# Kernel tuning notes

Hardware: AMD Instinct MI355X
Metric: run time of the kernel (lower is better)

Reference implementation:

```python
import jax, jax.numpy as jnp
import numpy as np

# dims: batch, seq_len, d_model, heads, head_dim, n_buckets
B, L, DM, H, DH, K = 4, 4096, 1024, 16, 64, 8
C = L // K            # chunk length after bucket sort (512); extra_len==0 for these dims
CS = 0.1              # cluster_score mixing weight


def setup_inputs() -> dict:
    key = jax.random.key(0)
    ks = jax.random.split(key, 12)
    s = 0.02
    def p(k, shape):
        return jax.random.normal(k, shape, jnp.float32) * s
    return {
        "inputs_q": jax.random.normal(ks[0], (B, L, DM), jnp.float32),
        "wq": p(ks[1], (DM, H, DH)), "bq": jnp.zeros((H, DH), jnp.float32),
        "wk": p(ks[2], (DM, H, DH)), "bk": jnp.zeros((H, DH), jnp.float32),
        "wv": p(ks[3], (DM, H, DH)), "bv": jnp.zeros((H, DH), jnp.float32),
        "w_shared": p(ks[4], (H, DH, K)),
        "w_qscore": p(ks[5], (H, DH, K)),
        "w_kscore": p(ks[6], (H, DH, K)),
        "wo": p(ks[7], (H, DH, DM)), "bo": jnp.zeros((DM,), jnp.float32),
    }


def reference(inputs_q, wq, bq, wk, bk, wv, bv, w_shared, w_qscore, w_kscore, wo, bo):
    scale = 1.0 / np.sqrt(DH)
    # QKV projections (DenseGeneral to (H, DH))
    q = jnp.einsum('bld,dhk->blhk', inputs_q, wq) + bq  # [B,L,H,DH]
    k = jnp.einsum('bld,dhk->blhk', inputs_q, wk) + bk
    v = jnp.einsum('bld,dhk->blhk', inputs_q, wv) + bv

    # learned linear cluster scores on stop-gradient q/k
    mix_q = (1.0 - CS) * w_shared + CS * w_qscore  # [H,DH,K]
    mix_k = (1.0 - CS) * w_shared + CS * w_kscore
    qs = jnp.einsum('blhd,hdk->blhk', jax.lax.stop_gradient(q), mix_q)  # [B,L,H,K]
    ksc = jnp.einsum('blhd,hdk->blhk', jax.lax.stop_gradient(k), mix_k)

    # bucket assignment = argmax learned score; per-(batch,head) stable sort by bucket id
    bq_id = jnp.argmax(qs, -1).transpose(0, 2, 1)   # [B,H,L]
    bk_id = jnp.argmax(ksc, -1).transpose(0, 2, 1)
    sort_q = jnp.argsort(bq_id, axis=-1)            # stable in jax
    sort_k = jnp.argsort(bk_id, axis=-1)

    qh = q.transpose(0, 2, 1, 3)  # [B,H,L,DH]
    kh = k.transpose(0, 2, 1, 3)
    vh = v.transpose(0, 2, 1, 3)
    sq = jnp.take_along_axis(qh, sort_q[..., None], axis=2).reshape(B, H, K, C, DH)
    sk = jnp.take_along_axis(kh, sort_k[..., None], axis=2).reshape(B, H, K, C, DH)
    sv = jnp.take_along_axis(vh, sort_k[..., None], axis=2).reshape(B, H, K, C, DH)

    # block attention within each bucket chunk
    logits = jnp.einsum('bhncd,bhned->bhnce', sq, sk) * scale  # [B,H,K,C,C]
    attn = jax.nn.softmax(logits, axis=-1)
    o = jnp.einsum('bhnce,bhned->bhncd', attn, sv).reshape(B, H, L, DH)

    # unsort back to original token order
    inv_q = jnp.argsort(sort_q, axis=-1)
    o = jnp.take_along_axis(o, inv_q[..., None], axis=2)  # [B,H,L,DH]
    o = o.transpose(0, 2, 1, 3)                            # [B,L,H,DH]

    out = jnp.einsum('blhd,hdo->blo', o, wo) + bo          # output projection

    # auxiliary load-balancing routing loss over buckets (extra_loss)
    p_q = jax.nn.softmax(qs, -1)
    p_k = jax.nn.softmax(ksc, -1)
    f_q = jax.nn.one_hot(jnp.argmax(qs, -1), K, dtype=qs.dtype)
    f_k = jax.nn.one_hot(jnp.argmax(ksc, -1), K, dtype=qs.dtype)
    lq = K * jnp.mean(jnp.sum(jnp.mean(f_q, 1) * jnp.mean(p_q, 1), -1))
    lk = K * jnp.mean(jnp.sum(jnp.mean(f_k, 1) * jnp.mean(p_k, 1), -1))
    extra_loss = 0.5 * (lq + lk)
    return out, extra_loss
```

## Files before the change

kernel.cpp:

```cpp
#include <hip/hip_runtime.h>
#include <hip/hip_bf16.h>

#define BB 4
#define LL 4096
#define DM 1024
#define HH 16
#define DHD 64
#define KB 8
#define BL 16384
#define FLAGCAP 131072

typedef __attribute__((ext_vector_type(8))) short short8;
typedef __attribute__((ext_vector_type(4))) short short4v;
typedef __attribute__((ext_vector_type(4))) float float4v;

#define MFMA16(A, Bx, C) __builtin_amdgcn_mfma_f32_16x16x32_bf16(A, Bx, C, 0, 0, 0)

static __device__ __forceinline__ short bf16s(float f) {
  __hip_bfloat16 h = __float2bfloat16(f);
  return *reinterpret_cast<short*>(&h);
}
static __device__ __forceinline__ float b2f(short s) {
  __hip_bfloat16 h = *reinterpret_cast<__hip_bfloat16*>(&s);
  return __bfloat162float(h);
}
static __device__ __forceinline__ void gl16(const void* g, void* l) {
  __builtin_amdgcn_global_load_lds(
      (const __attribute__((address_space(1))) void*)g,
      (__attribute__((address_space(3))) void*)l, 16, 0, 0);
}

__global__ __launch_bounds__(256) void xcvt(const float* __restrict__ x,
                                            __hip_bfloat16* __restrict__ xb) {
  int i = (blockIdx.x * 256 + threadIdx.x) * 8;
  float4 f0 = *reinterpret_cast<const float4*>(x + i);
  float4 f1 = *reinterpret_cast<const float4*>(x + i + 4);
  short8 o;
  o[0] = bf16s(f0.x); o[1] = bf16s(f0.y); o[2] = bf16s(f0.z); o[3] = bf16s(f0.w);
  o[4] = bf16s(f1.x); o[5] = bf16s(f1.y); o[6] = bf16s(f1.z); o[7] = bf16s(f1.w);
  *reinterpret_cast<short8*>(xb + i) = o;
}

__global__ __launch_bounds__(256) void prep_wt(const float* __restrict__ wq,
                                               const float* __restrict__ wk,
                                               const float* __restrict__ wv,
                                               const float* __restrict__ wo,
                                               __hip_bfloat16* __restrict__ wt_qkv,
                                               __hip_bfloat16* __restrict__ wt_o) {
  int blk = blockIdx.x;
  int s = blk >> 8;
  int rem = blk & 255;
  int k0 = (rem >> 4) * 64;
  int n0 = (rem & 15) * 64;
  const float* src = (s == 0) ? wq : (s == 1) ? wk : (s == 2) ? wv : wo;
  __hip_bfloat16* dst = (s < 3) ? (wt_qkv + (size_t)s * 1024 * 1024) : wt_o;
  __shared__ float ls[64][65];
  int t = threadIdx.x;
#pragma unroll
  for (int p = 0; p < 4; ++p) {
    int sid = p * 256 + t;
    int r = sid >> 4, c4 = sid & 15;
    float4 v = *reinterpret_cast<const float4*>(src + (size_t)(k0 + r) * 1024 + n0 + c4 * 4);
    ls[r][c4 * 4 + 0] = v.x; ls[r][c4 * 4 + 1] = v.y;
    ls[r][c4 * 4 + 2] = v.z; ls[r][c4 * 4 + 3] = v.w;
  }
  __syncthreads();
#pragma unroll
  for (int p = 0; p < 4; ++p) {
    int sid = p * 256 + t;
    int n = sid >> 4, kq = sid & 15;
    short4v pk;
#pragma unroll
    for (int j = 0; j < 4; ++j) pk[j] = bf16s(ls[kq * 4 + j][n]);
    *reinterpret_cast<short4v*>(dst + (size_t)(n0 + n) * 1024 + k0 + kq * 4) = pk;
  }
}

__global__ __launch_bounds__(256) void prep_wsc(const float* __restrict__ wq,
                                                const float* __restrict__ wk,
                                                const float* __restrict__ wsh,
                                                const float* __restrict__ wqs,
                                                const float* __restrict__ wks,
                                                const float* __restrict__ bq,
                                                const float* __restrict__ bk,
                                                double* __restrict__ wscg,
                                                double* __restrict__ bsc,
                                                __hip_bfloat16* __restrict__ whb,
                                                __hip_bfloat16* __restrict__ wmb) {
  int col = blockIdx.x;
  int side = col >> 7, h = (col >> 3) & 15, kk = col & 7;
  int g = side * 16 + h;
  const float* w = side ? wk : wq;
  const float* wscore = side ? wks : wqs;
  __shared__ double mix[64];
  int t = threadIdx.x;
  if (t < 64)
    mix[t] = 0.9 * (double)wsh[(h * 64 + t) * 8 + kk] +
             0.1 * (double)wscore[(h * 64 + t) * 8 + kk];
  __syncthreads();
#pragma unroll
  for (int p = 0; p < 4; ++p) {
    int d = p * 256 + t;
    double acc = 0.0;
    const float* wr = w + (size_t)d * 1024 + h * 64;
#pragma unroll
    for (int j = 0; j < 64; ++j) acc += (double)wr[j] * mix[j];
    wscg[((size_t)g * 1024 + d) * 8 + kk] = acc;
    short hi = bf16s((float)acc);
    short mid = bf16s((float)(acc - (double)b2f(hi)));
    *reinterpret_cast<short*>(whb + (size_t)col * 1024 + d) = hi;
    *reinterpret_cast<short*>(wmb + (size_t)col * 1024 + d) = mid;
  }
  if (t == 0) {
    const float* br = (side ? bk : bq) + h * 64;
    double acc = 0.0;
    for (int j = 0; j < 64; ++j) acc += (double)br[j] * mix[j];
    bsc[col] = acc;
  }
}

__global__ __launch_bounds__(256) void score_gemm(const float* __restrict__ x,
                                                  const __hip_bfloat16* __restrict__ whb,
                                                  const __hip_bfloat16* __restrict__ wmb,
                                                  const double* __restrict__ bsc,
                                                  float* __restrict__ S2) {
  __shared__ char sm[49152];
  int t = threadIdx.x;
  int m0 = blockIdx.x * 64;
  int n0 = blockIdx.y * 128;
  int lane = t & 63;
  int wu = __builtin_amdgcn_readfirstlane(t >> 6);
  int lm = lane & 15, quad = lane >> 4;
  int wmr = (wu & 1) * 32, wn = (wu >> 1) * 64;
  int rb = wu * 32, rr = lane >> 3, phys = lane & 7;
  float4v zero = {0.f, 0.f, 0.f, 0.f};
  float4v acc[2][4];
#pragma unroll
  for (int i = 0; i < 2; ++i)
#pragma unroll
    for (int j = 0; j < 4; ++j) acc[i][j] = zero;

  for (int k0 = 0; k0 < 1024; k0 += 64) {
    __syncthreads();
#pragma unroll
    for (int p = 0; p < 2; ++p) {
      int sid = p * 256 + t;
      int m = sid >> 3, kc = sid & 7;
      const float* ap = x + (size_t)(m0 + m) * 1024 + k0 + kc * 8;
      float4 f0 = *reinterpret_cast<const float4*>(ap);
      float4 f1 = *reinterpret_cast<const float4*>(ap + 4);
      float vv[8] = {f0.x, f0.y, f0.z, f0.w, f1.x, f1.y, f1.z, f1.w};
      short8 hi, lo;
#pragma unroll
      for (int e = 0; e < 8; ++e) {
        short h = bf16s(vv[e]);
        hi[e] = h;
        lo[e] = bf16s(vv[e] - b2f(h));
      }
      *reinterpret_cast<short8*>(sm + m * 128 + ((kc + m) & 7) * 16) = hi;
      *reinterpret_cast<short8*>(sm + 8192 + m * 128 + ((kc + m) & 7) * 16) = lo;
    }
#pragma unroll
    for (int p = 0; p < 4; ++p) {
      int row = rb + p * 8 + rr;
      int kc = (phys - row) & 7;
      gl16(whb + (size_t)(n0 + row) * 1024 + k0 + kc * 8, sm + 16384 + (rb + p * 8) * 128);
      gl16(wmb + (size_t)(n0 + row) * 1024 + k0 + kc * 8, sm + 32768 + (rb + p * 8) * 128);
    }
    __syncthreads();
#pragma unroll
    for (int kh = 0; kh < 2; ++kh) {
      short8 ah[2], al[2], bh[4], bm[4];
#pragma unroll
      for (int i = 0; i < 2; ++i) {
        int row = wmr + i * 16 + lm;
        int ph = ((kh * 4 + quad) + row) & 7;
        ah[i] = *reinterpret_cast<const short8*>(sm + row * 128 + ph * 16);
        al[i] = *reinterpret_cast<const short8*>(sm + 8192 + row * 128 + ph * 16);
      }
#pragma unroll
      for (int j = 0; j < 4; ++j) {
        int rn = wn + j * 16 + lm;
        int ph = ((kh * 4 + quad) + rn) & 7;
        bh[j] = *reinterpret_cast<const short8*>(sm + 16384 + rn * 128 + ph * 16);
        bm[j] = *reinterpret_cast<const short8*>(sm + 32768 + rn * 128 + ph * 16);
      }
#pragma unroll
      for (int i = 0; i < 2; ++i)
#pragma unroll
        for (int j = 0; j < 4; ++j) {
          acc[i][j] = MFMA16(ah[i], bh[j], acc[i][j]);
          acc[i][j] = MFMA16(ah[i], bm[j], acc[i][j]);
          acc[i][j] = MFMA16(al[i], bh[j], acc[i][j]);
        }
    }
  }

#pragma unroll
  for (int i = 0; i < 2; ++i)
#pragma unroll
    for (int j = 0; j < 4; ++j) {
      int n = n0 + wn + j * 16 + lm;
      float bias = (float)bsc[n];
#pragma unroll
      for (int r = 0; r < 4; ++r) {
        int row = m0 + wmr + i * 16 + quad * 4 + r;
        S2[(size_t)(n >> 3) * 131072 + row * 8 + (n & 7)] = acc[i][j][r] + bias;
      }
    }
}

__global__ __launch_bounds__(512) void bucket_kernel(const float* __restrict__ S2,
                                                     int* __restrict__ bid,
                                                     float* __restrict__ psumg,
                                                     int* __restrict__ flagcnt,
                                                     int* __restrict__ list) {
  int t = threadIdx.x;
  int lane = t & 63;
  int w = t >> 6;
  int T0 = blockIdx.x * 64;
  int tg = T0 + lane;
  int b = tg >> 12, l = tg & 4095;
#pragma unroll
  for (int gi = 0; gi < 4; ++gi) {
    int g = gi * 8 + w;
    const float* sp = S2 + (size_t)g * 131072 + tg * 8;
    float4 v0 = *reinterpret_cast<const float4*>(sp);
    float4 v1 = *reinterpret_cast<const float4*>(sp + 4);
    float v[8] = {v0.x, v0.y, v0.z, v0.w, v1.x, v1.y, v1.z, v1.w};
    float mx = v[0]; int am = 0;
#pragma unroll
    for (int j = 1; j < 8; ++j) { if (v[j] > mx) { mx = v[j]; am = j; } }
    float mx2 = -3.0e38f;
#pragma unroll
    for (int j = 0; j < 8; ++j) { if (j != am && v[j] > mx2) mx2 = v[j]; }
    int side = g >> 4, h = g & 15;
    int slab = (side * 4 + b) * 16 + h;
    bid[(slab << 12) | l] = am;
    if (mx - mx2 < 5e-4f) {
      int pos = atomicAdd(flagcnt, 1);
      if (pos < FLAGCAP) list[pos] = (slab << 12) | l;
    }
    float es = 0.f, e[8];
#pragma unroll
    for (int j = 0; j < 8; ++j) { e[j] = __expf(v[j] - mx); es += e[j]; }
    float inv = 1.f / es;
#pragma unroll
    for (int j = 0; j < 8; ++j) {
      float s = e[j] * inv;
      s += __shfl_xor(s, 1);  s += __shfl_xor(s, 2);  s += __shfl_xor(s, 4);
      s += __shfl_xor(s, 8);  s += __shfl_xor(s, 16); s += __shfl_xor(s, 32);
      if (lane == 0) atomicAdd(&psumg[slab * 8 + j], s);
    }
  }
}

__global__ __launch_bounds__(256) void refine_kernel(const float* __restrict__ x,
                                                     const double* __restrict__ wscg,
                                                     const double* __restrict__ bsc,
                                                     const int* __restrict__ flagcnt,
                                                     const int* __restrict__ list,
                                                     int* __restrict__ bid) {
  int lane = threadIdx.x & 63;
  int w = threadIdx.x >> 6;
  int cnt = flagcnt[0];
  if (cnt > FLAGCAP) cnt = FLAGCAP;
  for (int i = blockIdx.x * 4 + w; i < cnt; i += 1024) {
    int e = list[i];
    int slab = e >> 12, l = e & 4095;
    int side = slab >> 6, b = (slab >> 4) & 3, h = slab & 15;
    int g = side * 16 + h;
    int row = b * 4096 + l;
    double acc[8] = {0, 0, 0, 0, 0, 0, 0, 0};
    const float* xr = x + (size_t)row * 1024 + lane * 16;
    const double* wr = wscg + ((size_t)g * 1024 + lane * 16) * 8;
#pragma unroll
    for (int dd = 0; dd < 16; ++dd) {
      double xv = (double)xr[dd];
#pragma unroll
      for (int j = 0; j < 8; ++j) acc[j] += xv * wr[dd * 8 + j];
    }
#pragma unroll
    for (int j = 0; j < 8; ++j) {
      double v = acc[j];
      v += __shfl_xor(v, 32); v += __shfl_xor(v, 16); v += __shfl_xor(v, 8);
      v += __shfl_xor(v, 4);  v += __shfl_xor(v, 2);  v += __shfl_xor(v, 1);
      acc[j] = v + bsc[g * 8 + j];
    }
    if (lane == 0) {
      double mx = acc[0]; int am = 0;
#pragma unroll
      for (int j = 1; j < 8; ++j) { if (acc[j] > mx) { mx = acc[j]; am = j; } }
      bid[(slab << 12) | l] = am;
    }
  }
}

__global__ __launch_bounds__(256) void sort_kernel(const int* __restrict__ bid,
                                                   int* __restrict__ sortq,
                                                   int* __restrict__ sortk,
                                                   int* __restrict__ cntg) {
  int blk = blockIdx.x;
  int side = blk >> 6, b = (blk >> 4) & 3, h = blk & 15;
  const int* ids = bid + (((side * 4 + b) * 16 + h) << 12);
  int* outp = (side ? sortk : sortq) + ((b * 16 + h) << 12);
  __shared__ int cnt[8][257];
  __shared__ int base[8];
  int t = threadIdx.x;
  int loc[16];
  int hist[8] = {0, 0, 0, 0, 0, 0, 0, 0};
#pragma unroll
  for (int j = 0; j < 16; ++j) { loc[j] = ids[t * 16 + j] & 7; hist[loc[j]]++; }
#pragma unroll
  for (int k = 0; k < 8; ++k) cnt[k][t + 1] = hist[k];
  if (t < 8) cnt[t][0] = 0;
  __syncthreads();
  if (t < 8) {
    for (int i = 1; i <= 256; ++i) cnt[t][i] += cnt[t][i - 1];
  }
  __syncthreads();
  if (t == 0) {
    int run = 0;
    for (int k = 0; k < 8; ++k) { base[k] = run; run += cnt[k][256]; }
  }
  if (t < 8) cntg[((side * 4 + b) * 16 + h) * 8 + t] = cnt[t][256];
  __syncthreads();
#pragma unroll
  for (int j = 0; j < 16; ++j) {
    int k = loc[j];
    int before = 0;
#pragma unroll
    for (int i = 0; i < 16; ++i) before += (i < j && loc[i] == k) ? 1 : 0;
    int pos = base[k] + cnt[k][t] + before;
    outp[pos] = t * 16 + j;
  }
}

template <bool CBF16>
__global__ __launch_bounds__(256) void gemm_k(const __hip_bfloat16* __restrict__ A,
                                              const __hip_bfloat16* __restrict__ Bt,
                                              void* __restrict__ Cv,
                                              const float* __restrict__ b0,
                                              const float* __restrict__ b1,
                                              const float* __restrict__ b2,
                                              int nblk) {
  __shared__ char sm[32768];
  int t = threadIdx.x;
  int blk = blockIdx.x;
  int m0 = (blk / nblk) * 128;
  int n0 = (blk % nblk) * 128;
  int lane = t & 63;
  int wu = __builtin_amdgcn_readfirstlane(t >> 6);
  int lm = lane & 15, quad = lane >> 4;
  int wm = (wu & 1) * 64, wn = (wu >> 1) * 64;
  int rb = wu * 32, rr = lane >> 3, phys = lane & 7;
  float4v zero = {0.f, 0.f, 0.f, 0.f};
  float4v acc[4][4];
#pragma unroll
  for (int i = 0; i < 4; ++i)
#pragma unroll
    for (int j = 0; j < 4; ++j) acc[i][j] = zero;

  for (int k0 = 0; k0 < 1024; k0 += 64) {
    __syncthreads();
#pragma unroll
    for (int p = 0; p < 4; ++p) {
      int row = rb + p * 8 + rr;
      int kc = (phys - row) & 7;
      gl16(A + (size_t)(m0 + row) * 1024 + k0 + kc * 8, sm + (rb + p * 8) * 128);
      gl16(Bt + (size_t)(n0 + row) * 1024 + k0 + kc * 8, sm + 16384 + (rb + p * 8) * 128);
    }
    __syncthreads();
#pragma unroll
    for (int kh = 0; kh < 2; ++kh) {
      short8 af[4], bf[4];
#pragma unroll
      for (int i = 0; i < 4; ++i) {
        int row = wm + i * 16 + lm;
        int ph = ((kh * 4 + quad) + row) & 7;
        af[i] = *reinterpret_cast<const short8*>(sm + row * 128 + ph * 16);
        int rn = wn + i * 16 + lm;
        int phb = ((kh * 4 + quad) + rn) & 7;
        bf[i] = *reinterpret_cast<const short8*>(sm + 16384 + rn * 128 + phb * 16);
      }
#pragma unroll
      for (int i = 0; i < 4; ++i)
#pragma unroll
        for (int j = 0; j < 4; ++j) acc[i][j] = MFMA16(af[i], bf[j], acc[i][j]);
    }
  }

  if constexpr (CBF16) {
    int s = n0 >> 10, nnb = n0 & 1023;
    const float* bias = (s == 0) ? b0 : (s == 1) ? b1 : b2;
    __hip_bfloat16* C = (__hip_bfloat16*)Cv + (size_t)s * BL * 1024;
#pragma unroll
    for (int i = 0; i < 4; ++i)
#pragma unroll
      for (int j = 0; j < 4; ++j) {
        int nn = nnb + wn + j * 16 + lm;
        float bvx = bias[nn];
#pragma unroll
        for (int r = 0; r < 4; ++r) {
          int row = m0 + wm + i * 16 + quad * 4 + r;
          C[(size_t)row * 1024 + nn] = __float2bfloat16(acc[i][j][r] + bvx);
        }
      }
  } else {
    float* C = (float*)Cv;
#pragma unroll
    for (int i = 0; i < 4; ++i)
#pragma unroll
      for (int j = 0; j < 4; ++j) {
        int gn = n0 + wn + j * 16 + lm;
        float bvx = b0[gn];
#pragma unroll
        for (int r = 0; r < 4; ++r) {
          int row = m0 + wm + i * 16 + quad * 4 + r;
          C[(size_t)row * 1024 + gn] = acc[i][j][r] + bvx;
        }
      }
  }
}

__global__ __launch_bounds__(256) void vt_kernel(const __hip_bfloat16* __restrict__ vb,
                                                 const int* __restrict__ sortk,
                                                 __hip_bfloat16* __restrict__ vT) {
  int cid = blockIdx.x;
  int b = cid >> 7, h = (cid >> 3) & 15, n = cid & 7;
  int sbase = ((b * 16 + h) << 12) + n * 512;
  __shared__ __hip_bfloat16 ls[64][72];
  int t = threadIdx.x;
  for (int kt = 0; kt < 8; ++kt) {
    __syncthreads();
#pragma unroll
    for (int p = 0; p < 2; ++p) {
      int sid = p * 256 + t;
      int key = sid >> 3, kc = sid & 7;
      int tok = sortk[sbase + kt * 64 + key];
      short8 v = *reinterpret_cast<const short8*>(vb + ((size_t)(b * 4096 + tok) * 16 + h) * 64 + kc * 8);
      *reinterpret_cast<short8*>(&ls[key][kc * 8]) = v;
    }
    __syncthreads();
#pragma unroll
    for (int p = 0; p < 2; ++p) {
      int sid = p * 256 + t;
      int dim = sid >> 3, kc = sid & 7;
      short8 o;
#pragma unroll
      for (int j = 0; j < 8; ++j) o[j] = *reinterpret_cast<short*>(&ls[kc * 8 + j][dim]);
      *reinterpret_cast<short8*>(vT + ((size_t)cid * 64 + dim) * 512 + kt * 64 + kc * 8) = o;
    }
  }
}

__global__ __launch_bounds__(256) void attn_kernel(const __hip_bfloat16* __restrict__ qb,
                                                   const __hip_bfloat16* __restrict__ kb,
                                                   const __hip_bfloat16* __restrict__ vT,
                                                   const int* __restrict__ sortq,
                                                   const int* __restrict__ sortk,
                                                   __hip_bfloat16* __restrict__ ao) {
  __shared__ char sm[25600];
  int t = threadIdx.x;
  int lane = t & 63, w = t >> 6;
  int lm = lane & 15, quad = lane >> 4;
  int cid = blockIdx.x >> 3, qt = blockIdx.x & 7;
  int b = cid >> 7, h = (cid >> 3) & 15, n = cid & 7;
  int sbase = (b * 16 + h) << 12;
  int psOff = 16384 + w * 2304;

  int qtok = sortq[sbase + n * 512 + qt * 64 + w * 16 + lm];
  const __hip_bfloat16* qp = qb + ((size_t)(b * 4096 + qtok) * 16 + h) * 64 + quad * 8;
  short8 aq0 = *reinterpret_cast<const short8*>(qp);
  short8 aq1 = *reinterpret_cast<const short8*>(qp + 32);

  float4v zero = {0.f, 0.f, 0.f, 0.f};
  float4v accO[4];
#pragma unroll
  for (int i = 0; i < 4; ++i) accO[i] = zero;
  float lsum[4] = {0.f, 0.f, 0.f, 0.f};

  for (int kt = 0; kt < 8; ++kt) {
    __syncthreads();
#pragma unroll
    for (int p = 0; p < 2; ++p) {
      int sid = p * 256 + t;
      int row = sid >> 3, kc = sid & 7;
      int tok = sortk[sbase + n * 512 + kt * 64 + row];
      short8 kv = *reinterpret_cast<const short8*>(kb + ((size_t)(b * 4096 + tok) * 16 + h) * 64 + kc * 8);
      *reinterpret_cast<short8*>(sm + row * 128 + ((kc + row) & 7) * 16) = kv;
      short8 vv = *reinterpret_cast<const short8*>(vT + ((size_t)cid * 64 + row) * 512 + kt * 64 + kc * 8);
      *reinterpret_cast<short8*>(sm + 8192 + row * 128 + ((kc + row) & 7) * 16) = vv;
    }
    __syncthreads();
#pragma unroll
    for (int nt = 0; nt < 4; ++nt) {
      int key = nt * 16 + lm;
      int ph0 = (quad + key) & 7;
      int ph1 = (4 + quad + key) & 7;
      short8 bk0 = *reinterpret_cast<const short8*>(sm + key * 128 + ph0 * 16);
      short8 bk1 = *reinterpret_cast<const short8*>(sm + key * 128 + ph1 * 16);
      float4v S = zero;
      S = MFMA16(aq0, bk0, S);
      S = MFMA16(aq1, bk1, S);
#pragma unroll
      for (int r = 0; r < 4; ++r) {
        float e = __expf(S[r] * 0.125f);
        lsum[r] += e;
        *reinterpret_cast<short*>(sm + psOff + (quad * 4 + r) * 144 + key * 2) = bf16s(e);
      }
    }
    __builtin_amdgcn_s_waitcnt(0);
#pragma unroll
    for (int ks = 0; ks < 2; ++ks) {
      short8 ap = *reinterpret_cast<const short8*>(sm + psOff + lm * 144 + ks * 64 + quad * 16);
#pragma unroll
      for (int dt = 0; dt < 4; ++dt) {
        int dim = dt * 16 + lm;
        int ph = (ks * 4 + quad + dim) & 7;
        short8 bv = *reinterpret_cast<const short8*>(sm + 8192 + dim * 128 + ph * 16);
        accO[dt] = MFMA16(ap, bv, accO[dt]);
      }
    }
  }
#pragma unroll
  for (int r = 0; r < 4; ++r) {
    float l = lsum[r];
    l += __shfl_xor(l, 1); l += __shfl_xor(l, 2);
    l += __shfl_xor(l, 4); l += __shfl_xor(l, 8);
    lsum[r] = 1.f / l;
  }
#pragma unroll
  for (int dt = 0; dt < 4; ++dt)
#pragma unroll
    for (int r = 0; r < 4; ++r)
      *reinterpret_cast<short*>(sm + psOff + (quad * 4 + r) * 144 + (dt * 16 + lm) * 2) =
          bf16s(accO[dt][r] * lsum[r]);
  __builtin_amdgcn_s_waitcnt(0);
  int q2 = lane >> 2, c = lane & 3;
  int tok2 = sortq[sbase + n * 512 + qt * 64 + w * 16 + q2];
  __hip_bfloat16* op = ao + ((size_t)(b * 4096 + tok2) * 16 + h) * 64;
  short8 o0 = *reinterpret_cast<const short8*>(sm + psOff + q2 * 144 + c * 16);
  short8 o1 = *reinterpret_cast<const short8*>(sm + psOff + q2 * 144 + (c + 4) * 16);
  *reinterpret_cast<short8*>(op + c * 8) = o0;
  *reinterpret_cast<short8*>(op + (c + 4) * 8) = o1;
}

__global__ __launch_bounds__(1024) void loss_kernel(const int* __restrict__ cntg,
                                                    const float* __restrict__ psumg,
                                                    float* __restrict__ out) {
  int t = threadIdx.x;
  float term = ((float)cntg[t] * (1.f / 4096.f)) * (psumg[t] * (1.f / 4096.f));
#pragma unroll
  for (int o = 1; o < 64; o <<= 1) term += __shfl_xor(term, o);
  __shared__ float wsum[16];
  if ((t & 63) == 0) wsum[t >> 6] = term;
  __syncthreads();
  if (t == 0) {
    float s = 0.f;
    for (int i = 0; i < 16; ++i) s += wsum[i];
    out[16777216] = s * (1.f / 16.f);
  }
}

extern "C" void kernel_launch(void* const* d_in, const int* in_sizes, int n_in,
                              void* d_out, int out_size, void* d_ws, size_t ws_size,
                              hipStream_t stream) {
  (void)in_sizes; (void)n_in; (void)out_size; (void)ws_size;
  const float* x   = (const float*)d_in[0];
  const float* wq  = (const float*)d_in[1];
  const float* bq  = (const float*)d_in[2];
  const float* wk  = (const float*)d_in[3];
  const float* bk  = (const float*)d_in[4];
  const float* wv  = (const float*)d_in[5];
  const float* bv  = (const float*)d_in[6];
  const float* wsh = (const float*)d_in[7];
  const float* wqs = (const float*)d_in[8];
  const float* wks = (const float*)d_in[9];
  const float* wo  = (const float*)d_in[10];
  const float* bo  = (const float*)d_in[11];

  char* ws = (char*)d_ws;
  __hip_bfloat16* wt_qkv = (__hip_bfloat16*)(ws + 0);
  __hip_bfloat16* wt_o   = (__hip_bfloat16*)(ws + 6291456);
  double* wscg  = (double*)(ws + 8388608);
  double* bsc   = (double*)(ws + 10485760);
  __hip_bfloat16* qkv  = (__hip_bfloat16*)(ws + 10487808);
  __hip_bfloat16* whb = (__hip_bfloat16*)(ws + 109051904);
  __hip_bfloat16* wmb = (__hip_bfloat16*)(ws + 109576192);
  int* flagcnt = (int*)(ws + 110100480);
  int* list    = (int*)(ws + 110100736);
  __hip_bfloat16* attn = (__hip_bfloat16*)(ws + 111151104);
  float* S2 = (float*)(ws + 111151104);
  int* bid    = (int*)(ws + 144705536);
  int* sortq  = (int*)(ws + 146802688);
  int* sortk  = (int*)(ws + 147851264);
  float* psumg = (float*)(ws + 148899840);
  int* cntg    = (int*)(ws + 148903936);
  __hip_bfloat16* vT = (__hip_bfloat16*)d_out;
  __hip_bfloat16* xb = (__hip_bfloat16*)((char*)d_out + 33554432);
  float* out = (float*)d_out;

  hipMemsetAsync(psumg, 0, 8192, stream);
  hipMemsetAsync(flagcnt, 0, 4, stream);
  prep_wt<<<1024, 256, 0, stream>>>(wq, wk, wv, wo, wt_qkv, wt_o);
  prep_wsc<<<256, 256, 0, stream>>>(wq, wk, wsh, wqs, wks, bq, bk, wscg, bsc, whb, wmb);
  xcvt<<<8192, 256, 0, stream>>>(x, xb);
  score_gemm<<<dim3(256, 2), 256, 0, stream>>>(x, whb, wmb, bsc, S2);
  bucket_kernel<<<256, 512, 0, stream>>>(S2, bid, psumg, flagcnt, list);
  refine_kernel<<<256, 256, 0, stream>>>(x, wscg, bsc, flagcnt, list, bid);
  sort_kernel<<<128, 256, 0, stream>>>(bid, sortq, sortk, cntg);
  gemm_k<true><<<3072, 256, 0, stream>>>(xb, wt_qkv, qkv, bq, bk, bv, 24);
  vt_kernel<<<512, 256, 0, stream>>>(qkv + (size_t)2 * BL * 1024, sortk, vT);
  attn_kernel<<<4096, 256, 0, stream>>>(qkv, qkv + (size_t)BL * 1024, vT, sortq, sortk, attn);
  gemm_k<false><<<1024, 256, 0, stream>>>(attn, wt_o, (void*)out, bo, bo, bo, 8);
  loss_kernel<<<1, 1024, 0, stream>>>(cntg, psumg, out);
}
```

Before: 576.9 us.

## Replace GEMM with 256x256 double-buffered quadrant-pipelined MFMA kernel

New measurement: 559.2 us. -3.1%, faster.

```diff
diff --git a/kernel.cpp b/kernel.cpp
--- a/kernel.cpp
+++ b/kernel.cpp
@@ -337,89 +337,141 @@
 }
 
 template <bool CBF16>
-__global__ __launch_bounds__(256) void gemm_k(const __hip_bfloat16* __restrict__ A,
-                                              const __hip_bfloat16* __restrict__ Bt,
-                                              void* __restrict__ Cv,
-                                              const float* __restrict__ b0,
-                                              const float* __restrict__ b1,
-                                              const float* __restrict__ b2,
-                                              int nblk) {
-  __shared__ char sm[32768];
+__global__ __launch_bounds__(512, 2) void gemm256(const __hip_bfloat16* __restrict__ A,
+                                                  const __hip_bfloat16* __restrict__ Bt,
+                                                  void* __restrict__ Cv,
+                                                  const float* __restrict__ b0,
+                                                  const float* __restrict__ b1,
+                                                  const float* __restrict__ b2,
+                                                  int nblk) {
+  __shared__ char sm[131072];
   int t = threadIdx.x;
   int blk = blockIdx.x;
-  int m0 = (blk / nblk) * 128;
-  int n0 = (blk % nblk) * 128;
+  int m0 = (blk / nblk) * 256;
+  int n0 = (blk % nblk) * 256;
   int lane = t & 63;
   int wu = __builtin_amdgcn_readfirstlane(t >> 6);
   int lm = lane & 15, quad = lane >> 4;
-  int wm = (wu & 1) * 64, wn = (wu >> 1) * 64;
-  int rb = wu * 32, rr = lane >> 3, phys = lane & 7;
+  int rr = lane >> 3, phys = lane & 7;
+  int wrow = (wu & 1) * 64;
+  int wcol = (wu >> 1) * 32;
+
+  constexpr int QM[4] = {0, 0, 1, 1};
+  constexpr int QN[4] = {0, 1, 1, 0};
+
+  auto STAGE = [&](char* bufn, int j, int kS) {
+    const int mat = (j == 1 || j == 2) ? 1 : 0;
+    const int hm = (j >= 2) ? 1 : 0;
+    const __hip_bfloat16* src = mat ? Bt : A;
+    int gb = mat ? n0 : m0;
+    char* lb = bufn + mat * 32768 + hm * 16384;
+#pragma unroll
+    for (int i = 0; i < 2; ++i) {
+      int r = hm * 128 + (wu * 2 + i) * 8 + rr;
+      int kc = (phys - r) & 7;
+      gl16(src + (size_t)(gb + r) * 1024 + kS + kc * 8, lb + (wu * 2 + i) * 1024);
+    }
+  };
+
+#pragma unroll
+  for (int j = 0; j < 4; ++j) STAGE(sm, j, 0);
+
   float4v zero = {0.f, 0.f, 0.f, 0.f};
-  float4v acc[4][4];
-#pragma unroll
-  for (int i = 0; i < 4; ++i)
-#pragma unroll
-    for (int j = 0; j < 4; ++j) acc[i][j] = zero;
-
-  for (int k0 = 0; k0 < 1024; k0 += 64) {
-    __syncthreads();
-#pragma unroll
-    for (int p = 0; p < 4; ++p) {
-      int row = rb + p * 8 + rr;
-      int kc = (phys - row) & 7;
-      gl16(A + (size_t)(m0 + row) * 1024 + k0 + kc * 8, sm + (rb + p * 8) * 128);
-      gl16(Bt + (size_t)(n0 + row) * 1024 + k0 + kc * 8, sm + 16384 + (rb + p * 8) * 128);
-    }
-    __syncthreads();
-#pragma unroll
-    for (int kh = 0; kh < 2; ++kh) {
-      short8 af[4], bf[4];
-#pragma unroll
-      for (int i = 0; i < 4; ++i) {
-        int row = wm + i * 16 + lm;
-        int ph = ((kh * 4 + quad) + row) & 7;
-        af[i] = *reinterpret_cast<const short8*>(sm + row * 128 + ph * 16);
-        int rn = wn + i * 16 + lm;
-        int phb = ((kh * 4 + quad) + rn) & 7;
-        bf[i] = *reinterpret_cast<const short8*>(sm + 16384 + rn * 128 + phb * 16);
-      }
-#pragma unroll
-      for (int i = 0; i < 4; ++i)
-#pragma unroll
-        for (int j = 0; j < 4; ++j) acc[i][j] = MFMA16(af[i], bf[j], acc[i][j]);
-    }
-  }
+  float4v acc[4][4][2];
+#pragma unroll
+  for (int q = 0; q < 4; ++q)
+#pragma unroll
+    for (int mi = 0; mi < 4; ++mi)
+#pragma unroll
+      for (int ni = 0; ni < 2; ++ni) acc[q][mi][ni] = zero;
+
+  short8 a[4][2], b[2][2];
+  auto READA = [&](const char* bc, int qm) {
+#pragma unroll
+    for (int mi = 0; mi < 4; ++mi) {
+      int row = qm * 128 + wrow + mi * 16 + lm;
+#pragma unroll
+      for (int ks = 0; ks < 2; ++ks) {
+        int ph = ((ks * 4 + quad) + row) & 7;
+        a[mi][ks] = *reinterpret_cast<const short8*>(bc + row * 128 + ph * 16);
+      }
+    }
+  };
+  auto READB = [&](const char* bc, int qn) {
+#pragma unroll
+    for (int ni = 0; ni < 2; ++ni) {
+      int rn = qn * 128 + wcol + ni * 16 + lm;
+#pragma unroll
+      for (int ks = 0; ks < 2; ++ks) {
+        int ph = ((ks * 4 + quad) + rn) & 7;
+        b[ni][ks] = *reinterpret_cast<const short8*>(bc + 32768 + rn * 128 + ph * 16);
+      }
+    }
+  };
+
+#pragma unroll 1
+  for (int kt = 0; kt < 16; ++kt) {
+    char* bc = sm + ((kt & 1) << 16);
+    char* bn = sm + (((kt & 1) ^ 1) << 16);
+    int kS = (kt < 15) ? (kt + 1) * 64 : 960;
+#pragma unroll
+    for (int j = 0; j < 4; ++j) {
+      if (j < 3) {
+        asm volatile("s_waitcnt vmcnt(4)" ::: "memory");
+        __builtin_amdgcn_s_barrier();
+      }
+      if (j == 0) { READA(bc, 0); READB(bc, 0); }
+      else if (j == 1) { READB(bc, 1); }
+      else if (j == 2) { READA(bc, 1); }
+      else { READB(bc, 0); }
+      STAGE(bn, j, kS);
+      __builtin_amdgcn_s_setprio(1);
+#pragma unroll
+      for (int mi = 0; mi < 4; ++mi)
+#pragma unroll
+        for (int ni = 0; ni < 2; ++ni)
+#pragma unroll
+          for (int ks = 0; ks < 2; ++ks)
+            acc[j][mi][ni] = MFMA16(a[mi][ks], b[ni][ks], acc[j][mi][ni]);
+      __builtin_amdgcn_s_setprio(0);
+    }
+  }
+  asm volatile("s_waitcnt vmcnt(0)" ::: "memory");
 
   if constexpr (CBF16) {
-    int s = n0 >> 10, nnb = n0 & 1023;
-    const float* bias = (s == 0) ? b0 : (s == 1) ? b1 : b2;
-    __hip_bfloat16* C = (__hip_bfloat16*)Cv + (size_t)s * BL * 1024;
-#pragma unroll
-    for (int i = 0; i < 4; ++i)
-#pragma unroll
-      for (int j = 0; j < 4; ++j) {
-        int nn = nnb + wn + j * 16 + lm;
-        float bvx = bias[nn];
-#pragma unroll
-        for (int r = 0; r < 4; ++r) {
-          int row = m0 + wm + i * 16 + quad * 4 + r;
-          C[(size_t)row * 1024 + nn] = __float2bfloat16(acc[i][j][r] + bvx);
+#pragma unroll
+    for (int j = 0; j < 4; ++j)
+#pragma unroll
+      for (int mi = 0; mi < 4; ++mi)
+#pragma unroll
+        for (int ni = 0; ni < 2; ++ni) {
+          int nn = n0 + QN[j] * 128 + wcol + ni * 16 + lm;
+          int s = nn >> 10, nnb = nn & 1023;
+          const float* bias = (s == 0) ? b0 : (s == 1) ? b1 : b2;
+          float bvx = bias[nnb];
+          __hip_bfloat16* C = (__hip_bfloat16*)Cv + (size_t)s * BL * 1024;
+#pragma unroll
+          for (int r = 0; r < 4; ++r) {
+            int row = m0 + QM[j] * 128 + wrow + mi * 16 + quad * 4 + r;
+            C[(size_t)row * 1024 + nnb] = __float2bfloat16(acc[j][mi][ni][r] + bvx);
+          }
         }
-      }
   } else {
     float* C = (float*)Cv;
 #pragma unroll
-    for (int i = 0; i < 4; ++i)
-#pragma unroll
-      for (int j = 0; j < 4; ++j) {
-        int gn = n0 + wn + j * 16 + lm;
-        float bvx = b0[gn];
-#pragma unroll
-        for (int r = 0; r < 4; ++r) {
-          int row = m0 + wm + i * 16 + quad * 4 + r;
-          C[(size_t)row * 1024 + gn] = acc[i][j][r] + bvx;
+    for (int j = 0; j < 4; ++j)
+#pragma unroll
+      for (int mi = 0; mi < 4; ++mi)
+#pragma unroll
+        for (int ni = 0; ni < 2; ++ni) {
+          int nn = n0 + QN[j] * 128 + wcol + ni * 16 + lm;
+          float bvx = b0[nn];
+#pragma unroll
+          for (int r = 0; r < 4; ++r) {
+            int row = m0 + QM[j] * 128 + wrow + mi * 16 + quad * 4 + r;
+            C[(size_t)row * 1024 + nn] = acc[j][mi][ni][r] + bvx;
+          }
         }
-      }
   }
 }
 
@@ -610,9 +662,9 @@
   bucket_kernel<<<256, 512, 0, stream>>>(S2, bid, psumg, flagcnt, list);
   refine_kernel<<<256, 256, 0, stream>>>(x, wscg, bsc, flagcnt, list, bid);
   sort_kernel<<<128, 256, 0, stream>>>(bid, sortq, sortk, cntg);
-  gemm_k<true><<<3072, 256, 0, stream>>>(xb, wt_qkv, qkv, bq, bk, bv, 24);
+  gemm256<true><<<768, 512, 0, stream>>>(xb, wt_qkv, qkv, bq, bk, bv, 12);
   vt_kernel<<<512, 256, 0, stream>>>(qkv + (size_t)2 * BL * 1024, sortk, vT);
   attn_kernel<<<4096, 256, 0, stream>>>(qkv, qkv + (size_t)BL * 1024, vT, sortq, sortk, attn);
-  gemm_k<false><<<1024, 256, 0, stream>>>(attn, wt_o, (void*)out, bo, bo, bo, 8);
+  gemm256<false><<<256, 512, 0, stream>>>(attn, wt_o, (void*)out, bo, bo, bo, 4);
   loss_kernel<<<1, 1024, 0, stream>>>(cntg, psumg, out);
 }
```
